# Kernel tuning notes

Measured on AMD Instinct MI355X. Metric: run time of the kernel, lower is better.

## Reference

```python
import jax, jax.numpy as jnp
import numpy as np

TARGET_DIM = 50257
BATCH = 4096


def setup_inputs() -> dict:
    key = jax.random.key(0)
    k1, k2 = jax.random.split(key)
    out = jax.random.normal(k1, (BATCH, TARGET_DIM), dtype=jnp.float32)
    label = jax.random.randint(k2, (BATCH,), 0, TARGET_DIM, dtype=jnp.int64)
    return {"out": out, "label": label}


def reference(out, label):
    # Original: loss = -2 * out * one_hot(label); return loss.mean()
    # one_hot zeros out everything except out[i, label[i]], and .mean()
    # divides by batch * target_dim. Equivalent single-pass gather:
    B, V = out.shape
    gathered = jnp.take_along_axis(out, label[:, None].astype(jnp.int32), axis=1)[:, 0]  # [B]
    return (-2.0 * gathered).sum() / (B * V)
```

## Files before the change

### kernel.cpp

```cpp
#include <hip/hip_runtime.h>


__global__ __launch_bounds__(1024)
void LinearClassification_71167608095256_kernel(const float* __restrict__ outm,
                                                const int* __restrict__ lab32,
                                                float* __restrict__ res,
                                                int B, long long V) {
    const int tid      = threadIdx.x;
    const int nthreads = blockDim.x;
    const int lane     = tid & 63;
    const int wave     = tid >> 6;
    const int nwaves   = (nthreads + 63) >> 6;

    __shared__ int    s_nz[16];
    __shared__ int    s_is64;
    __shared__ double s_part[16];

    int nonzero = 0;
    for (int j = 2 * tid + 1; j < B; j += 2 * nthreads)
        nonzero |= (lab32[j] != 0);
    unsigned long long ball = __ballot(nonzero);
    if (lane == 0) s_nz[wave] = (ball != 0ull) ? 1 : 0;
    __syncthreads();
    if (tid == 0) {
        int nz = 0;
        for (int w = 0; w < nwaves; ++w) nz |= s_nz[w];
        s_is64 = (nz == 0);
    }
    __syncthreads();
    const bool is64 = (s_is64 != 0);

    double acc = 0.0;
    for (int i = tid; i < B; i += nthreads) {
        const long long idx = (long long)(is64 ? lab32[2 * i] : lab32[i]);
        acc += (double)outm[(long long)i * V + idx];
    }

    #pragma unroll
    for (int off = 32; off > 0; off >>= 1)
        acc += __shfl_down(acc, off, 64);
    if (lane == 0) s_part[wave] = acc;
    __syncthreads();
    if (tid == 0) {
        double t = 0.0;
        for (int w = 0; w < nwaves; ++w) t += s_part[w];
        res[0] = (float)(-2.0 * t / ((double)B * (double)V));
    }
}

extern "C" void kernel_launch(void* const* d_in, const int* in_sizes, int n_in,
                              void* d_out, int out_size, void* d_ws, size_t ws_size,
                              hipStream_t stream) {
    const float* outm = (const float*)d_in[0];
    const int*   lab  = (const int*)d_in[1];
    float*       res  = (float*)d_out;

    const int B = in_sizes[1];
    const long long V = (long long)in_sizes[0] / B;

    LinearClassification_71167608095256_kernel<<<1, 1024, 0, stream>>>(
        outm, lab, res, B, V);
}
```

Baseline: 9.730 us.

## Spread gather across many blocks with last-block atomic reduction

Replaces the single 1024-thread block with one thread per row across B/256 blocks. Each block reduces its rows and publishes a partial sum, and the last block to arrive, found through an atomic counter, sums all partials. The label-width check now reads only the first 64 odd entries, and the gather is issued speculatively before that check so the loads overlap. This spreads the latency-bound scattered loads over many CUs, at the cost of an extra memset launch and an atomic handoff between blocks.

```diff
diff --git a/kernel.cpp b/kernel.cpp
--- a/kernel.cpp
+++ b/kernel.cpp
@@ -1,39 +1,50 @@
 #include <hip/hip_runtime.h>
 
 
-__global__ __launch_bounds__(1024)
+#define BLOCK 256
+
+__global__ __launch_bounds__(BLOCK)
 void LinearClassification_71167608095256_kernel(const float* __restrict__ outm,
                                                 const int* __restrict__ lab32,
                                                 float* __restrict__ res,
-                                                int B, long long V) {
-    const int tid      = threadIdx.x;
-    const int nthreads = blockDim.x;
-    const int lane     = tid & 63;
-    const int wave     = tid >> 6;
-    const int nwaves   = (nthreads + 63) >> 6;
+                                                unsigned int* __restrict__ counter,
+                                                double* __restrict__ partials,
+                                                int B, long long V, int nblocks) {
+    const int tid  = threadIdx.x;
+    const int gtid = blockIdx.x * BLOCK + tid;
+    const int lane = tid & 63;
+    const int wave = tid >> 6;
 
-    __shared__ int    s_nz[16];
     __shared__ int    s_is64;
-    __shared__ double s_part[16];
+    __shared__ double s_part[BLOCK / 64];
 
     int nonzero = 0;
-    for (int j = 2 * tid + 1; j < B; j += 2 * nthreads)
-        nonzero |= (lab32[j] != 0);
-    unsigned long long ball = __ballot(nonzero);
-    if (lane == 0) s_nz[wave] = (ball != 0ull) ? 1 : 0;
-    __syncthreads();
-    if (tid == 0) {
-        int nz = 0;
-        for (int w = 0; w < nwaves; ++w) nz |= s_nz[w];
-        s_is64 = (nz == 0);
+    if (wave == 0) {
+        int j = 2 * lane + 1;
+        if (j < B) nonzero = (lab32[j] != 0);
+    }
+
+    int   labv = 0;
+    float gv   = 0.0f;
+    if (gtid < B) {
+        labv = lab32[gtid];
+        gv   = outm[(long long)gtid * V + (long long)labv];
+    }
+
+    if (wave == 0) {
+        unsigned long long ball = __ballot(nonzero);
+        if (lane == 0) s_is64 = (ball == 0ull) ? 1 : 0;
     }
     __syncthreads();
-    const bool is64 = (s_is64 != 0);
 
     double acc = 0.0;
-    for (int i = tid; i < B; i += nthreads) {
-        const long long idx = (long long)(is64 ? lab32[2 * i] : lab32[i]);
-        acc += (double)outm[(long long)i * V + idx];
+    if (gtid < B) {
+        if (!s_is64) {
+            acc = (double)gv;
+        } else {
+            const long long idx = (long long)lab32[2 * gtid];
+            acc = (double)outm[(long long)gtid * V + idx];
+        }
     }
 
     #pragma unroll
@@ -41,10 +52,27 @@
         acc += __shfl_down(acc, off, 64);
     if (lane == 0) s_part[wave] = acc;
     __syncthreads();
+
     if (tid == 0) {
         double t = 0.0;
-        for (int w = 0; w < nwaves; ++w) t += s_part[w];
-        res[0] = (float)(-2.0 * t / ((double)B * (double)V));
+        #pragma unroll
+        for (int w = 0; w < BLOCK / 64; ++w) t += s_part[w];
+
+        __hip_atomic_store((unsigned long long*)&partials[blockIdx.x],
+                           __builtin_bit_cast(unsigned long long, t),
+                           __ATOMIC_RELEASE, __HIP_MEMORY_SCOPE_AGENT);
+        unsigned int old = __hip_atomic_fetch_add(counter, 1u, __ATOMIC_ACQ_REL,
+                                                  __HIP_MEMORY_SCOPE_AGENT);
+        if (old == (unsigned int)(nblocks - 1)) {
+            double t2 = 0.0;
+            for (int b = 0; b < nblocks; ++b) {
+                unsigned long long u = __hip_atomic_load(
+                    (unsigned long long*)&partials[b],
+                    __ATOMIC_ACQUIRE, __HIP_MEMORY_SCOPE_AGENT);
+                t2 += __builtin_bit_cast(double, u);
+            }
+            res[0] = (float)(-2.0 * t2 / ((double)B * (double)V));
+        }
     }
 }
 
@@ -57,7 +85,12 @@
 
     const int B = in_sizes[1];
     const long long V = (long long)in_sizes[0] / B;
+    const int nblocks = (B + BLOCK - 1) / BLOCK;
 
-    LinearClassification_71167608095256_kernel<<<1, 1024, 0, stream>>>(
-        outm, lab, res, B, V);
+    unsigned int* counter  = (unsigned int*)d_ws;
+    double*       partials = (double*)((char*)d_ws + 64);
+
+    hipMemsetAsync(counter, 0, sizeof(unsigned int), stream);
+    LinearClassification_71167608095256_kernel<<<nblocks, BLOCK, 0, stream>>>(
+        outm, lab, res, counter, partials, B, V, nblocks);
 }
```

New measurement: 15.90 us. +63.4%, slower.
